# Kernel tuning notes

Hardware: AMD Instinct MI355X
Metric: run time of the kernel (lower is better)

Reference implementation:

```python
import jax, jax.numpy as jnp
import numpy as np

B, S, T, C, H = 16, 64, 4096, 512, 8
D = C // H
NEG = jnp.float32(-1e30)


def setup_inputs() -> dict:
    key = jax.random.key(0)
    ks = jax.random.split(key, 12)
    x = jax.random.normal(ks[0], (1, C, 1), dtype=jnp.float32)
    eh = jax.random.normal(ks[1], (B, C, T), dtype=jnp.float32)
    # ragged shot boundaries -> fixed (B, S) start/end arrays, end > start
    bounds = jnp.sort(jax.random.randint(ks[2], (B, S + 1), 0, T), axis=-1)
    shot_starts = bounds[:, :-1].astype(jnp.int32)
    shot_ends = jnp.maximum(bounds[:, 1:], shot_starts + 1).astype(jnp.int32)
    sc = 1.0 / np.sqrt(C)
    Wq = jax.random.normal(ks[3], (C, C), dtype=jnp.float32) * sc
    bq = jnp.zeros((C,), dtype=jnp.float32)
    Wk = jax.random.normal(ks[4], (C, C), dtype=jnp.float32) * sc
    bk = jnp.zeros((C,), dtype=jnp.float32)
    Wv = jax.random.normal(ks[5], (C, C), dtype=jnp.float32) * sc
    bv = jnp.zeros((C,), dtype=jnp.float32)
    Wp = jax.random.normal(ks[6], (C, C), dtype=jnp.float32) * sc
    bp = jnp.zeros((C,), dtype=jnp.float32)
    return {"x": x, "encoder_hidden_states": eh, "shot_starts": shot_starts,
            "shot_ends": shot_ends, "Wq": Wq, "bq": bq, "Wk": Wk, "bk": bk,
            "Wv": Wv, "bv": bv, "Wp": Wp, "bp": bp}


def reference(x, encoder_hidden_states, shot_starts, shot_ends,
              Wq, bq, Wk, bk, Wv, bv, Wp, bp):
    scale = 1.0 / np.sqrt(D)
    # 1x1 conv == pointwise matmul over channels
    q = (Wq @ x[0] + bq[:, None])            # (C, 1)
    k = jnp.einsum('oc,bct->bot', Wk, encoder_hidden_states) + bk[None, :, None]
    v = jnp.einsum('oc,bct->bot', Wv, encoder_hidden_states) + bv[None, :, None]
    qh = q.reshape(H, D) * scale             # (H, D) single query per head
    kh = k.reshape(B, H, D, T)               # (B, H, D, T)
    vh = v.reshape(B, H, D, T).transpose(0, 1, 3, 2)  # (B, H, T, D)
    att = jnp.einsum('hd,bhdt->bht', qh, kh)          # (B, H, T)
    pos = jnp.arange(T)
    seg = (pos[None, None, :] >= shot_starts[:, :, None]) & \
          (pos[None, None, :] < shot_ends[:, :, None])  # (B, S, T)
    logits = jnp.where(seg[:, :, None, :], att[:, None, :, :], NEG)  # (B,S,H,T)
    p = jax.nn.softmax(logits, axis=-1)
    out = jnp.einsum('bsht,bhtd->bshd', p, vh)        # (B, S, H, D)
    out = out.reshape(B * S, C)
    out = out @ Wp.T + bp                              # proj (1x1 conv)
    return out[:, :, None]                             # (B*S, C, 1)
```

## Files before the change

kernel.cpp:

```cpp
#include <hip/hip_runtime.h>
#include <cstdint>
#include <cstddef>

#define B_ 16
#define S_ 64
#define T_ 4096
#define C_ 512
#define H_ 8

#define WS_QKT     0
#define WS_QB      4096
#define WS_ATT     8192
#define WS_WSUM    532480
#define WS_ATTNOUT 4726784

__global__ void k_prep(const float* __restrict__ x, const float* __restrict__ Wq,
                       const float* __restrict__ bq, const float* __restrict__ Wk,
                       const float* __restrict__ bk, float* __restrict__ qkT,
                       float* __restrict__ qb) {
  __shared__ float xs[C_];
  __shared__ float part[4][64];
  __shared__ float qh[64];
  int tid = threadIdx.x;
  int h = blockIdx.x;
  xs[tid] = x[tid];
  xs[tid + 256] = x[tid + 256];
  __syncthreads();
  int d = tid & 63, pp = tid >> 6;
  const float* wrow = Wq + (size_t)(h * 64 + d) * C_ + pp * 128;
  const float* xp = xs + pp * 128;
  float s = 0.f;
#pragma unroll 4
  for (int c = 0; c < 128; ++c) s += wrow[c] * xp[c];
  part[pp][d] = s;
  __syncthreads();
  if (tid < 64) {
    float qv = part[0][tid] + part[1][tid] + part[2][tid] + part[3][tid] +
               bq[h * 64 + tid];
    qh[tid] = qv * 0.125f;
  }
  __syncthreads();
  if (tid == 0) {
    float sb = 0.f;
    for (int dd = 0; dd < 64; ++dd) sb += qh[dd] * bk[h * 64 + dd];
    qb[h] = sb;
  }
  for (int c = tid; c < C_; c += 256) {
    float s2 = 0.f;
#pragma unroll 8
    for (int dd = 0; dd < 64; ++dd)
      s2 += qh[dd] * Wk[(size_t)(h * 64 + dd) * C_ + c];
    qkT[c * 8 + h] = s2;
  }
}

__global__ __launch_bounds__(256, 4) void k_att(
    const float* __restrict__ eh, const float* __restrict__ qkT,
    const float* __restrict__ qb, float* __restrict__ att) {
  __shared__ float qks[C_ * 8];
  __shared__ float part[4 * 8 * 64];
  int tid = threadIdx.x;
  int tl = tid & 63, cg = tid >> 6;
  int b = blockIdx.y;
  int t0 = blockIdx.x * 64;
#pragma unroll
  for (int i = 0; i < 16; ++i) qks[tid + i * 256] = qkT[tid + i * 256];
  __syncthreads();
  const float* ehp = eh + ((size_t)b * C_ + (size_t)cg * 128) * T_ + t0 + tl;
  float acc[8];
#pragma unroll
  for (int h = 0; h < 8; ++h) acc[h] = 0.f;
#pragma unroll 4
  for (int j = 0; j < 128; ++j) {
    float e = ehp[(size_t)j * T_];
    const float4 q0 = *(const float4*)&qks[(cg * 128 + j) * 8];
    const float4 q1 = *(const float4*)&qks[(cg * 128 + j) * 8 + 4];
    acc[0] += q0.x * e; acc[1] += q0.y * e; acc[2] += q0.z * e; acc[3] += q0.w * e;
    acc[4] += q1.x * e; acc[5] += q1.y * e; acc[6] += q1.z * e; acc[7] += q1.w * e;
  }
#pragma unroll
  for (int h = 0; h < 8; ++h) part[(cg * 8 + h) * 64 + tl] = acc[h];
  __syncthreads();
#pragma unroll
  for (int i = 0; i < 2; ++i) {
    int idx = tid + i * 256;
    int h = idx >> 6, tt = idx & 63;
    float v = part[(0 * 8 + h) * 64 + tt] + part[(1 * 8 + h) * 64 + tt] +
              part[(2 * 8 + h) * 64 + tt] + part[(3 * 8 + h) * 64 + tt] + qb[h];
    att[((size_t)b * H_ + h) * T_ + t0 + tt] = v;
  }
}

__global__ __launch_bounds__(256, 4) void k_wsum(
    const float* __restrict__ eh, const float* __restrict__ att,
    const int* __restrict__ starts, const int* __restrict__ ends,
    float* __restrict__ wsum) {
  __shared__ float pl[8 * 64];
  __shared__ float ms[8], li[8];
  int tid = threadIdx.x;
  int n = blockIdx.x;
  int b = n >> 6;
  int start = starts[n], end = ends[n];
  int h = tid >> 5, tl = tid & 31;
  const float* ah = att + ((size_t)b * H_ + h) * T_;

  float mloc = -3.0e38f;
  for (int t = start + tl; t < end; t += 32) mloc = fmaxf(mloc, ah[t]);
#pragma unroll
  for (int off = 16; off > 0; off >>= 1)
    mloc = fmaxf(mloc, __shfl_xor(mloc, off, 32));
  float lloc = 0.f;
  for (int t = start + tl; t < end; t += 32) lloc += __expf(ah[t] - mloc);
#pragma unroll
  for (int off = 16; off > 0; off >>= 1) lloc += __shfl_xor(lloc, off, 32);
  if (tl == 0) { ms[h] = mloc; li[h] = 1.f / lloc; }

  float acc0[8], acc1[8];
#pragma unroll
  for (int i = 0; i < 8; ++i) { acc0[i] = 0.f; acc1[i] = 0.f; }
  const float* e0p = eh + ((size_t)b * C_ + tid) * T_;
  const float* e1p = e0p + (size_t)256 * T_;
  __syncthreads();

  int tbeg = start & ~3;
  for (int t0 = tbeg; t0 < end; t0 += 64) {
#pragma unroll
    for (int i = 0; i < 2; ++i) {
      int idx = tid + i * 256;
      int hh = idx >> 6;
      int tt = t0 + (idx & 63);
      float pv = 0.f;
      if (tt >= start && tt < end)
        pv = __expf(att[((size_t)b * H_ + hh) * T_ + tt] - ms[hh]) * li[hh];
      pl[idx] = pv;
    }
    __syncthreads();
    int tend = (t0 + 64 < end) ? t0 + 64 : end;
    for (int t = t0; t < tend; t += 4) {
      float4 e0 = *(const float4*)(e0p + t);
      float4 e1 = *(const float4*)(e1p + t);
      int base = t - t0;
#pragma unroll
      for (int hh = 0; hh < 8; ++hh) {
        const float4 p = *(const float4*)&pl[hh * 64 + base];
        acc0[hh] += p.x * e0.x + p.y * e0.y + p.z * e0.z + p.w * e0.w;
        acc1[hh] += p.x * e1.x + p.y * e1.y + p.z * e1.z + p.w * e1.w;
      }
    }
    __syncthreads();
  }
  float* wp = wsum + (size_t)n * (H_ * C_);
#pragma unroll
  for (int hh = 0; hh < 8; ++hh) {
    wp[hh * C_ + tid] = acc0[hh];
    wp[hh * C_ + 256 + tid] = acc1[hh];
  }
}

__global__ __launch_bounds__(256, 4) void k_gemm(
    const float* __restrict__ A, long aRow, long aColPerY,
    const float* __restrict__ Bm, const float* __restrict__ bias,
    float* __restrict__ Cc) {
  __shared__ float As[32 * 36];
  __shared__ float Bs[64 * 36];
  int tid = threadIdx.x;
  int n0 = blockIdx.x * 32;
  int y = blockIdx.y;
  const float* Abase = A + (size_t)n0 * aRow + (size_t)y * aColPerY;
  const float* Bbase = Bm + (size_t)(y * 64) * C_;
  int tx = tid & 15, ty = tid >> 4;
  float acc[2][4];
#pragma unroll
  for (int a = 0; a < 2; ++a)
#pragma unroll
    for (int bb = 0; bb < 4; ++bb) acc[a][bb] = 0.f;
  for (int k0 = 0; k0 < 512; k0 += 32) {
#pragma unroll
    for (int i = 0; i < 4; ++i) {
      int idx = tid + i * 256;
      int r = idx >> 5, cc = idx & 31;
      As[r * 36 + cc] = Abase[(size_t)r * aRow + k0 + cc];
    }
#pragma unroll
    for (int i = 0; i < 8; ++i) {
      int idx = tid + i * 256;
      int r = idx >> 5, cc = idx & 31;
      Bs[r * 36 + cc] = Bbase[(size_t)r * C_ + k0 + cc];
    }
    __syncthreads();
#pragma unroll
    for (int k = 0; k < 32; k += 4) {
      const float4 a0 = *(const float4*)&As[(ty * 2 + 0) * 36 + k];
      const float4 a1 = *(const float4*)&As[(ty * 2 + 1) * 36 + k];
#pragma unroll
      for (int bb = 0; bb < 4; ++bb) {
        const float4 bv = *(const float4*)&Bs[(tx * 4 + bb) * 36 + k];
        acc[0][bb] += a0.x * bv.x + a0.y * bv.y + a0.z * bv.z + a0.w * bv.w;
        acc[1][bb] += a1.x * bv.x + a1.y * bv.y + a1.z * bv.z + a1.w * bv.w;
      }
    }
    __syncthreads();
  }
#pragma unroll
  for (int a = 0; a < 2; ++a) {
    int nn = n0 + ty * 2 + a;
    float4 o;
    o.x = acc[a][0] + bias[y * 64 + tx * 4 + 0];
    o.y = acc[a][1] + bias[y * 64 + tx * 4 + 1];
    o.z = acc[a][2] + bias[y * 64 + tx * 4 + 2];
    o.w = acc[a][3] + bias[y * 64 + tx * 4 + 3];
    *(float4*)&Cc[(size_t)nn * C_ + y * 64 + tx * 4] = o;
  }
}

extern "C" void kernel_launch(void* const* d_in, const int* in_sizes, int n_in,
                              void* d_out, int out_size, void* d_ws,
                              size_t ws_size, hipStream_t stream) {
  const float* x = (const float*)d_in[0];
  const float* eh = (const float*)d_in[1];
  const int* shot_starts = (const int*)d_in[2];
  const int* shot_ends = (const int*)d_in[3];
  const float* Wq = (const float*)d_in[4];
  const float* bq = (const float*)d_in[5];
  const float* Wk = (const float*)d_in[6];
  const float* bk = (const float*)d_in[7];
  const float* Wv = (const float*)d_in[8];
  const float* bv = (const float*)d_in[9];
  const float* Wp = (const float*)d_in[10];
  const float* bp = (const float*)d_in[11];
  float* out = (float*)d_out;

  float* ws = (float*)d_ws;
  float* qkT = ws + WS_QKT;
  float* qb = ws + WS_QB;
  float* att = ws + WS_ATT;
  float* wsum = ws + WS_WSUM;
  float* attnout = ws + WS_ATTNOUT;

  k_prep<<<8, 256, 0, stream>>>(x, Wq, bq, Wk, bk, qkT, qb);
  k_att<<<dim3(T_ / 64, B_), 256, 0, stream>>>(eh, qkT, qb, att);
  k_wsum<<<B_ * S_, 256, 0, stream>>>(eh, att, shot_starts, shot_ends, wsum);
  k_gemm<<<dim3(32, 8), 256, 0, stream>>>(wsum, (long)(H_ * C_), (long)C_, Wv,
                                          bv, attnout);
  k_gemm<<<dim3(32, 8), 256, 0, stream>>>(attnout, (long)C_, 0L, Wp, bp, out);
}
```

Measured before the change: 396.7 us.

## Restructure weighted sum into time-window blocks with atomics and retile GEMMs

```diff
diff --git a/kernel.cpp b/kernel.cpp
--- a/kernel.cpp
+++ b/kernel.cpp
@@ -10,9 +10,11 @@
 
 #define WS_QKT     0
 #define WS_QB      4096
-#define WS_ATT     8192
-#define WS_WSUM    532480
-#define WS_ATTNOUT 4726784
+#define WS_MS      8192
+#define WS_LI      16384
+#define WS_ATT     24576
+#define WS_WSUM    548864
+#define WS_ATTNOUT 4743168
 
 __global__ void k_prep(const float* __restrict__ x, const float* __restrict__ Wq,
                        const float* __restrict__ bq, const float* __restrict__ Wk,
@@ -22,7 +24,7 @@
   __shared__ float part[4][64];
   __shared__ float qh[64];
   int tid = threadIdx.x;
-  int h = blockIdx.x;
+  int cs = blockIdx.x, h = blockIdx.y;
   xs[tid] = x[tid];
   xs[tid + 256] = x[tid + 256];
   __syncthreads();
@@ -40,12 +42,13 @@
     qh[tid] = qv * 0.125f;
   }
   __syncthreads();
-  if (tid == 0) {
+  if (cs == 0 && tid == 0) {
     float sb = 0.f;
     for (int dd = 0; dd < 64; ++dd) sb += qh[dd] * bk[h * 64 + dd];
     qb[h] = sb;
   }
-  for (int c = tid; c < C_; c += 256) {
+  if (tid < 64) {
+    int c = cs * 64 + tid;
     float s2 = 0.f;
 #pragma unroll 8
     for (int dd = 0; dd < 64; ++dd)
@@ -57,26 +60,24 @@
 __global__ __launch_bounds__(256, 4) void k_att(
     const float* __restrict__ eh, const float* __restrict__ qkT,
     const float* __restrict__ qb, float* __restrict__ att) {
-  __shared__ float qks[C_ * 8];
   __shared__ float part[4 * 8 * 64];
   int tid = threadIdx.x;
-  int tl = tid & 63, cg = tid >> 6;
+  int tl = tid & 63;
+  int cg = __builtin_amdgcn_readfirstlane(tid >> 6);
   int b = blockIdx.y;
   int t0 = blockIdx.x * 64;
-#pragma unroll
-  for (int i = 0; i < 16; ++i) qks[tid + i * 256] = qkT[tid + i * 256];
-  __syncthreads();
   const float* ehp = eh + ((size_t)b * C_ + (size_t)cg * 128) * T_ + t0 + tl;
+  const float* qp = qkT + (size_t)cg * 128 * 8;
   float acc[8];
 #pragma unroll
   for (int h = 0; h < 8; ++h) acc[h] = 0.f;
 #pragma unroll 4
   for (int j = 0; j < 128; ++j) {
     float e = ehp[(size_t)j * T_];
-    const float4 q0 = *(const float4*)&qks[(cg * 128 + j) * 8];
-    const float4 q1 = *(const float4*)&qks[(cg * 128 + j) * 8 + 4];
-    acc[0] += q0.x * e; acc[1] += q0.y * e; acc[2] += q0.z * e; acc[3] += q0.w * e;
-    acc[4] += q1.x * e; acc[5] += q1.y * e; acc[6] += q1.z * e; acc[7] += q1.w * e;
+    acc[0] += qp[j * 8 + 0] * e; acc[1] += qp[j * 8 + 1] * e;
+    acc[2] += qp[j * 8 + 2] * e; acc[3] += qp[j * 8 + 3] * e;
+    acc[4] += qp[j * 8 + 4] * e; acc[5] += qp[j * 8 + 5] * e;
+    acc[6] += qp[j * 8 + 6] * e; acc[7] += qp[j * 8 + 7] * e;
   }
 #pragma unroll
   for (int h = 0; h < 8; ++h) part[(cg * 8 + h) * 64 + tl] = acc[h];
@@ -91,19 +92,16 @@
   }
 }
 
-__global__ __launch_bounds__(256, 4) void k_wsum(
-    const float* __restrict__ eh, const float* __restrict__ att,
-    const int* __restrict__ starts, const int* __restrict__ ends,
-    float* __restrict__ wsum) {
-  __shared__ float pl[8 * 64];
-  __shared__ float ms[8], li[8];
+__global__ void k_stats(const float* __restrict__ att,
+                        const int* __restrict__ starts,
+                        const int* __restrict__ ends, float* __restrict__ ms,
+                        float* __restrict__ li) {
   int tid = threadIdx.x;
   int n = blockIdx.x;
   int b = n >> 6;
   int start = starts[n], end = ends[n];
   int h = tid >> 5, tl = tid & 31;
   const float* ah = att + ((size_t)b * H_ + h) * T_;
-
   float mloc = -3.0e38f;
   for (int t = start + tl; t < end; t += 32) mloc = fmaxf(mloc, ah[t]);
 #pragma unroll
@@ -113,103 +111,138 @@
   for (int t = start + tl; t < end; t += 32) lloc += __expf(ah[t] - mloc);
 #pragma unroll
   for (int off = 16; off > 0; off >>= 1) lloc += __shfl_xor(lloc, off, 32);
-  if (tl == 0) { ms[h] = mloc; li[h] = 1.f / lloc; }
-
-  float acc0[8], acc1[8];
-#pragma unroll
-  for (int i = 0; i < 8; ++i) { acc0[i] = 0.f; acc1[i] = 0.f; }
-  const float* e0p = eh + ((size_t)b * C_ + tid) * T_;
+  if (tl == 0) { ms[n * 8 + h] = mloc; li[n * 8 + h] = 1.f / lloc; }
+}
+
+__global__ __launch_bounds__(256, 4) void k_wsum_win(
+    const float* __restrict__ eh, const float* __restrict__ att,
+    const float* __restrict__ ms, const float* __restrict__ li,
+    const int* __restrict__ starts, const int* __restrict__ ends,
+    float* __restrict__ wsum) {
+  __shared__ float pl[8 * 64];
+  __shared__ int sseg[64], eseg[64];
+  int tid = threadIdx.x;
+  int b = blockIdx.y;
+  int w0 = blockIdx.x * 64;
+  if (tid < 64) {
+    sseg[tid] = starts[b * 64 + tid];
+    eseg[tid] = ends[b * 64 + tid];
+  }
+  __syncthreads();
+  int slo = 64, shi = 0;
+  for (int s = 0; s < 64; ++s) {
+    if (eseg[s] > w0 && sseg[s] < w0 + 64) {
+      if (s < slo) slo = s;
+      shi = s + 1;
+    }
+  }
+  const float* e0p = eh + ((size_t)b * C_ + tid) * T_ + w0;
   const float* e1p = e0p + (size_t)256 * T_;
-  __syncthreads();
-
-  int tbeg = start & ~3;
-  for (int t0 = tbeg; t0 < end; t0 += 64) {
+  for (int s = slo; s < shi; ++s) {
+    int n = b * 64 + s;
+    int st = sseg[s], en = eseg[s];
+    int Ilo = st > w0 ? st : w0;
+    int Ihi = en < w0 + 64 ? en : w0 + 64;
 #pragma unroll
     for (int i = 0; i < 2; ++i) {
       int idx = tid + i * 256;
-      int hh = idx >> 6;
-      int tt = t0 + (idx & 63);
+      int h = idx >> 6;
+      int t = w0 + (idx & 63);
       float pv = 0.f;
-      if (tt >= start && tt < end)
-        pv = __expf(att[((size_t)b * H_ + hh) * T_ + tt] - ms[hh]) * li[hh];
+      if (t >= Ilo && t < Ihi)
+        pv = __expf(att[((size_t)b * H_ + h) * T_ + t] - ms[n * 8 + h]) *
+             li[n * 8 + h];
       pl[idx] = pv;
     }
     __syncthreads();
-    int tend = (t0 + 64 < end) ? t0 + 64 : end;
-    for (int t = t0; t < tend; t += 4) {
-      float4 e0 = *(const float4*)(e0p + t);
-      float4 e1 = *(const float4*)(e1p + t);
-      int base = t - t0;
-#pragma unroll
-      for (int hh = 0; hh < 8; ++hh) {
-        const float4 p = *(const float4*)&pl[hh * 64 + base];
-        acc0[hh] += p.x * e0.x + p.y * e0.y + p.z * e0.z + p.w * e0.w;
-        acc1[hh] += p.x * e1.x + p.y * e1.y + p.z * e1.z + p.w * e1.w;
-      }
-    }
-    __syncthreads();
-  }
-  float* wp = wsum + (size_t)n * (H_ * C_);
-#pragma unroll
-  for (int hh = 0; hh < 8; ++hh) {
-    wp[hh * C_ + tid] = acc0[hh];
-    wp[hh * C_ + 256 + tid] = acc1[hh];
+    float acc0[8], acc1[8];
+#pragma unroll
+    for (int h = 0; h < 8; ++h) { acc0[h] = 0.f; acc1[h] = 0.f; }
+    int jlo = (Ilo - w0) & ~3, jhi = Ihi - w0;
+    for (int j = jlo; j < jhi; j += 4) {
+      float4 e0 = *(const float4*)(e0p + j);
+      float4 e1 = *(const float4*)(e1p + j);
+#pragma unroll
+      for (int h = 0; h < 8; ++h) {
+        const float4 p = *(const float4*)&pl[h * 64 + j];
+        acc0[h] += p.x * e0.x + p.y * e0.y + p.z * e0.z + p.w * e0.w;
+        acc1[h] += p.x * e1.x + p.y * e1.y + p.z * e1.z + p.w * e1.w;
+      }
+    }
+    float* wp = wsum + (size_t)n * (H_ * C_);
+    bool inner = (st >= w0) && (en <= w0 + 64);
+    if (inner) {
+#pragma unroll
+      for (int h = 0; h < 8; ++h) {
+        wp[h * C_ + tid] = acc0[h];
+        wp[h * C_ + 256 + tid] = acc1[h];
+      }
+    } else {
+#pragma unroll
+      for (int h = 0; h < 8; ++h) {
+        atomicAdd(&wp[h * C_ + tid], acc0[h]);
+        atomicAdd(&wp[h * C_ + 256 + tid], acc1[h]);
+      }
+    }
+    __syncthreads();
   }
 }
 
 __global__ __launch_bounds__(256, 4) void k_gemm(
-    const float* __restrict__ A, long aRow, long aColPerY,
-    const float* __restrict__ Bm, const float* __restrict__ bias,
+    const float* __restrict__ A, int aStride, int aColPerH,
+    const float* __restrict__ W, const float* __restrict__ bias,
     float* __restrict__ Cc) {
-  __shared__ float As[32 * 36];
-  __shared__ float Bs[64 * 36];
-  int tid = threadIdx.x;
-  int n0 = blockIdx.x * 32;
-  int y = blockIdx.y;
-  const float* Abase = A + (size_t)n0 * aRow + (size_t)y * aColPerY;
-  const float* Bbase = Bm + (size_t)(y * 64) * C_;
-  int tx = tid & 15, ty = tid >> 4;
-  float acc[2][4];
-#pragma unroll
-  for (int a = 0; a < 2; ++a)
-#pragma unroll
-    for (int bb = 0; bb < 4; ++bb) acc[a][bb] = 0.f;
-  for (int k0 = 0; k0 < 512; k0 += 32) {
-#pragma unroll
-    for (int i = 0; i < 4; ++i) {
-      int idx = tid + i * 256;
-      int r = idx >> 5, cc = idx & 31;
-      As[r * 36 + cc] = Abase[(size_t)r * aRow + k0 + cc];
-    }
-#pragma unroll
-    for (int i = 0; i < 8; ++i) {
-      int idx = tid + i * 256;
-      int r = idx >> 5, cc = idx & 31;
-      Bs[r * 36 + cc] = Bbase[(size_t)r * C_ + k0 + cc];
-    }
-    __syncthreads();
-#pragma unroll
-    for (int k = 0; k < 32; k += 4) {
-      const float4 a0 = *(const float4*)&As[(ty * 2 + 0) * 36 + k];
-      const float4 a1 = *(const float4*)&As[(ty * 2 + 1) * 36 + k];
-#pragma unroll
-      for (int bb = 0; bb < 4; ++bb) {
-        const float4 bv = *(const float4*)&Bs[(tx * 4 + bb) * 36 + k];
-        acc[0][bb] += a0.x * bv.x + a0.y * bv.y + a0.z * bv.z + a0.w * bv.w;
-        acc[1][bb] += a1.x * bv.x + a1.y * bv.y + a1.z * bv.z + a1.w * bv.w;
-      }
-    }
-    __syncthreads();
-  }
-#pragma unroll
-  for (int a = 0; a < 2; ++a) {
-    int nn = n0 + ty * 2 + a;
+  __shared__ float As[64 * 65];
+  __shared__ float Cs[64 * 33];
+  int tid = threadIdx.x;
+  int lane = tid & 63;
+  int wv = __builtin_amdgcn_readfirstlane(tid >> 6);
+  int n0 = blockIdx.x * 64, j0 = blockIdx.y * 32;
+  const float* Ab = A + (size_t)n0 * aStride + (size_t)(j0 >> 6) * aColPerH;
+  const float* Wb = W + (size_t)(j0 + wv * 8) * C_;
+  float acc[8];
+#pragma unroll
+  for (int jj = 0; jj < 8; ++jj) acc[jj] = 0.f;
+  int sn = tid >> 4, sk = (tid & 15) * 4;
+  for (int k0 = 0; k0 < 512; k0 += 64) {
+#pragma unroll
+    for (int r = 0; r < 4; ++r) {
+      int nn = r * 16 + sn;
+      float4 a = *(const float4*)&Ab[(size_t)nn * aStride + k0 + sk];
+      As[(sk + 0) * 65 + nn] = a.x;
+      As[(sk + 1) * 65 + nn] = a.y;
+      As[(sk + 2) * 65 + nn] = a.z;
+      As[(sk + 3) * 65 + nn] = a.w;
+    }
+    __syncthreads();
+#pragma unroll 4
+    for (int kk = 0; kk < 64; kk += 4) {
+      float a0 = As[(kk + 0) * 65 + lane];
+      float a1 = As[(kk + 1) * 65 + lane];
+      float a2 = As[(kk + 2) * 65 + lane];
+      float a3 = As[(kk + 3) * 65 + lane];
+      const float* wr = Wb + k0 + kk;
+#pragma unroll
+      for (int jj = 0; jj < 8; ++jj) {
+        const float* w4 = wr + (size_t)jj * C_;
+        acc[jj] += w4[0] * a0 + w4[1] * a1 + w4[2] * a2 + w4[3] * a3;
+      }
+    }
+    __syncthreads();
+  }
+#pragma unroll
+  for (int jj = 0; jj < 8; ++jj) Cs[lane * 33 + wv * 8 + jj] = acc[jj];
+  __syncthreads();
+#pragma unroll
+  for (int r = 0; r < 2; ++r) {
+    int idx = tid + r * 256;
+    int n = idx >> 3, j4 = (idx & 7) * 4;
     float4 o;
-    o.x = acc[a][0] + bias[y * 64 + tx * 4 + 0];
-    o.y = acc[a][1] + bias[y * 64 + tx * 4 + 1];
-    o.z = acc[a][2] + bias[y * 64 + tx * 4 + 2];
-    o.w = acc[a][3] + bias[y * 64 + tx * 4 + 3];
-    *(float4*)&Cc[(size_t)nn * C_ + y * 64 + tx * 4] = o;
+    o.x = Cs[n * 33 + j4 + 0] + bias[j0 + j4 + 0];
+    o.y = Cs[n * 33 + j4 + 1] + bias[j0 + j4 + 1];
+    o.z = Cs[n * 33 + j4 + 2] + bias[j0 + j4 + 2];
+    o.w = Cs[n * 33 + j4 + 3] + bias[j0 + j4 + 3];
+    *(float4*)&Cc[(size_t)(n0 + n) * C_ + j0 + j4] = o;
   }
 }
 
@@ -233,14 +266,19 @@
   float* ws = (float*)d_ws;
   float* qkT = ws + WS_QKT;
   float* qb = ws + WS_QB;
+  float* ms = ws + WS_MS;
+  float* li = ws + WS_LI;
   float* att = ws + WS_ATT;
   float* wsum = ws + WS_WSUM;
   float* attnout = ws + WS_ATTNOUT;
 
-  k_prep<<<8, 256, 0, stream>>>(x, Wq, bq, Wk, bk, qkT, qb);
+  hipMemsetAsync(wsum, 0, (size_t)1024 * H_ * C_ * sizeof(float), stream);
+  k_prep<<<dim3(8, 8), 256, 0, stream>>>(x, Wq, bq, Wk, bk, qkT, qb);
   k_att<<<dim3(T_ / 64, B_), 256, 0, stream>>>(eh, qkT, qb, att);
-  k_wsum<<<B_ * S_, 256, 0, stream>>>(eh, att, shot_starts, shot_ends, wsum);
-  k_gemm<<<dim3(32, 8), 256, 0, stream>>>(wsum, (long)(H_ * C_), (long)C_, Wv,
-                                          bv, attnout);
-  k_gemm<<<dim3(32, 8), 256, 0, stream>>>(attnout, (long)C_, 0L, Wp, bp, out);
-}
+  k_stats<<<B_ * S_, 256, 0, stream>>>(att, shot_starts, shot_ends, ms, li);
+  k_wsum_win<<<dim3(T_ / 64, B_), 256, 0, stream>>>(eh, att, ms, li,
+                                                    shot_starts, shot_ends,
+                                                    wsum);
+  k_gemm<<<dim3(16, 16), 256, 0, stream>>>(wsum, H_ * C_, C_, Wv, bv, attnout);
+  k_gemm<<<dim3(16, 16), 256, 0, stream>>>(attnout, C_, 0, Wp, bp, out);
+}
```

Result: slower. 467.6 us (+17.9%).
